# Optimization experiments

Measured on AMD Instinct MI355X. Metric: run time of the kernel, lower is better.

## Reference

```python
import jax, jax.numpy as jnp
import numpy as np

NUM_SKILLS = 50000
HIDDEN = 64
B, T = 8192, 1024
EPS = 1e-6


def setup_inputs() -> dict:
    key = jax.random.key(0)
    ks = jax.random.split(key, 8)
    X = jax.random.randint(ks[0], (B,), 0, NUM_SKILLS)
    y = jax.random.randint(ks[1], (B, T), 0, 2, dtype=jnp.int32)
    embed = jax.random.normal(ks[2], (NUM_SKILLS, HIDDEN), jnp.float32)
    bound = 1.0 / np.sqrt(HIDDEN)
    W0 = jax.random.uniform(ks[3], (HIDDEN, HIDDEN), jnp.float32, -bound, bound)
    b0 = jnp.zeros((HIDDEN,), jnp.float32)
    W1 = jax.random.uniform(ks[4], (HIDDEN, HIDDEN), jnp.float32, -bound, bound)
    b1 = jnp.zeros((HIDDEN,), jnp.float32)
    Wout = jax.random.uniform(ks[5], (HIDDEN, 4), jnp.float32, -bound, bound)
    bout = jnp.zeros((4,), jnp.float32)
    return {"X": X, "y": y, "embed": embed, "W0": W0, "b0": b0,
            "W1": W1, "b1": b1, "Wout": Wout, "bout": bout}


def reference(X, y, embed, W0, b0, W1, b1, Wout, bout):
    # Per-student BKT params from embedding + 2-layer MLP + sigmoid, clamped
    h = embed[X]                                   # (B, H)
    h = jax.nn.relu(h @ W0 + b0)
    h = jax.nn.relu(h @ W1 + b1)
    params = jnp.clip(jax.nn.sigmoid(h @ Wout + bout), EPS, 1.0 - EPS)  # (B, 4)
    l, g, s, prior = params[:, 0], params[:, 1], params[:, 2], params[:, 3]

    def step(latent, y_t):
        true_correct = jnp.where(y_t == -1, 0, y_t)
        correct = latent * (1.0 - s) + (1.0 - latent) * g
        k_t1 = latent * (1.0 - s) / correct
        k_t0 = latent * s / (latent * s + (1.0 - latent) * (1.0 - g))
        k_t = jnp.where(true_correct > 0.5, k_t1, k_t0)
        next_latent = jnp.clip(k_t + (1.0 - k_t) * l, EPS, 1.0 - EPS)
        return next_latent, (correct, latent)

    _, (corrects, latents) = jax.lax.scan(step, prior, y.T)  # scan over T
    return corrects.T, latents.T                            # (B, T) each
```

## Files before the change

kernel.cpp:

```cpp
#include <hip/hip_runtime.h>

#define TSTEPS 1024
#define NROWS  8192
#define CLEN   16
#define KEPS   1e-6f

__device__ __forceinline__ float clampP(float x) {
    return fminf(fmaxf(x, KEPS), 1.f - KEPS);
}
__device__ __forceinline__ float sigm(float v) {
    return 1.0f / (1.0f + __expf(-v));
}

__global__ __launch_bounds__(256) void bkt_params_v4(
    const int* __restrict__ X, const float* __restrict__ embed,
    const float* __restrict__ W0, const float* __restrict__ b0,
    const float* __restrict__ W1, const float* __restrict__ b1,
    const float* __restrict__ Wout, const float* __restrict__ bout,
    float4* __restrict__ params)
{
    const int lane    = threadIdx.x & 63;
    const int wid     = threadIdx.x >> 6;
    const int rowbase = blockIdx.x * 16 + wid * 4;

    __shared__ float sh[4][4][64];
    float (*shw)[64] = sh[wid];

    #pragma unroll
    for (int rs = 0; rs < 4; ++rs) {
        const int skill = X[rowbase + rs];
        shw[rs][lane] = embed[(size_t)skill * 64 + lane];
    }
    __syncthreads();

    float a0 = b0[lane], a1 = a0, a2 = a0, a3 = a0;
    #pragma unroll
    for (int k4 = 0; k4 < 16; ++k4) {
        const float4 e0 = *(const float4*)&shw[0][k4 * 4];
        const float4 e1 = *(const float4*)&shw[1][k4 * 4];
        const float4 e2 = *(const float4*)&shw[2][k4 * 4];
        const float4 e3 = *(const float4*)&shw[3][k4 * 4];
        const float w0 = W0[(k4 * 4 + 0) * 64 + lane];
        const float w1 = W0[(k4 * 4 + 1) * 64 + lane];
        const float w2 = W0[(k4 * 4 + 2) * 64 + lane];
        const float w3 = W0[(k4 * 4 + 3) * 64 + lane];
        a0 = fmaf(e0.x, w0, a0); a0 = fmaf(e0.y, w1, a0); a0 = fmaf(e0.z, w2, a0); a0 = fmaf(e0.w, w3, a0);
        a1 = fmaf(e1.x, w0, a1); a1 = fmaf(e1.y, w1, a1); a1 = fmaf(e1.z, w2, a1); a1 = fmaf(e1.w, w3, a1);
        a2 = fmaf(e2.x, w0, a2); a2 = fmaf(e2.y, w1, a2); a2 = fmaf(e2.z, w2, a2); a2 = fmaf(e2.w, w3, a2);
        a3 = fmaf(e3.x, w0, a3); a3 = fmaf(e3.y, w1, a3); a3 = fmaf(e3.z, w2, a3); a3 = fmaf(e3.w, w3, a3);
    }
    __syncthreads();
    shw[0][lane] = fmaxf(a0, 0.f);
    shw[1][lane] = fmaxf(a1, 0.f);
    shw[2][lane] = fmaxf(a2, 0.f);
    shw[3][lane] = fmaxf(a3, 0.f);
    __syncthreads();

    a0 = b1[lane]; a1 = a0; a2 = a0; a3 = a0;
    #pragma unroll
    for (int k4 = 0; k4 < 16; ++k4) {
        const float4 e0 = *(const float4*)&shw[0][k4 * 4];
        const float4 e1 = *(const float4*)&shw[1][k4 * 4];
        const float4 e2 = *(const float4*)&shw[2][k4 * 4];
        const float4 e3 = *(const float4*)&shw[3][k4 * 4];
        const float w0 = W1[(k4 * 4 + 0) * 64 + lane];
        const float w1 = W1[(k4 * 4 + 1) * 64 + lane];
        const float w2 = W1[(k4 * 4 + 2) * 64 + lane];
        const float w3 = W1[(k4 * 4 + 3) * 64 + lane];
        a0 = fmaf(e0.x, w0, a0); a0 = fmaf(e0.y, w1, a0); a0 = fmaf(e0.z, w2, a0); a0 = fmaf(e0.w, w3, a0);
        a1 = fmaf(e1.x, w0, a1); a1 = fmaf(e1.y, w1, a1); a1 = fmaf(e1.z, w2, a1); a1 = fmaf(e1.w, w3, a1);
        a2 = fmaf(e2.x, w0, a2); a2 = fmaf(e2.y, w1, a2); a2 = fmaf(e2.z, w2, a2); a2 = fmaf(e2.w, w3, a2);
        a3 = fmaf(e3.x, w0, a3); a3 = fmaf(e3.y, w1, a3); a3 = fmaf(e3.z, w2, a3); a3 = fmaf(e3.w, w3, a3);
    }
    const float h0r = fmaxf(a0, 0.f), h1r = fmaxf(a1, 0.f);
    const float h2r = fmaxf(a2, 0.f), h3r = fmaxf(a3, 0.f);

    const float4 wo = ((const float4*)Wout)[lane];
    float p[4][4];
    p[0][0] = h0r * wo.x; p[0][1] = h0r * wo.y; p[0][2] = h0r * wo.z; p[0][3] = h0r * wo.w;
    p[1][0] = h1r * wo.x; p[1][1] = h1r * wo.y; p[1][2] = h1r * wo.z; p[1][3] = h1r * wo.w;
    p[2][0] = h2r * wo.x; p[2][1] = h2r * wo.y; p[2][2] = h2r * wo.z; p[2][3] = h2r * wo.w;
    p[3][0] = h3r * wo.x; p[3][1] = h3r * wo.y; p[3][2] = h3r * wo.z; p[3][3] = h3r * wo.w;
    #pragma unroll
    for (int off = 32; off >= 1; off >>= 1) {
        #pragma unroll
        for (int rs = 0; rs < 4; ++rs)
            #pragma unroll
            for (int c = 0; c < 4; ++c)
                p[rs][c] += __shfl_xor(p[rs][c], off, 64);
    }
    const float4 bo = *(const float4*)bout;
    float v0 = (lane == 0) ? p[0][0] : (lane == 1) ? p[1][0] : (lane == 2) ? p[2][0] : p[3][0];
    float v1 = (lane == 0) ? p[0][1] : (lane == 1) ? p[1][1] : (lane == 2) ? p[2][1] : p[3][1];
    float v2 = (lane == 0) ? p[0][2] : (lane == 1) ? p[1][2] : (lane == 2) ? p[2][2] : p[3][2];
    float v3 = (lane == 0) ? p[0][3] : (lane == 1) ? p[1][3] : (lane == 2) ? p[2][3] : p[3][3];
    if (lane < 4) {
        float4 r;
        r.x = clampP(sigm(v0 + bo.x));
        r.y = clampP(sigm(v1 + bo.y));
        r.z = clampP(sigm(v2 + bo.z));
        r.w = clampP(sigm(v3 + bo.w));
        params[rowbase + lane] = r;
    }
}

__global__ __launch_bounds__(256) void bkt_scan_v4(
    const int* __restrict__ y, const float4* __restrict__ params,
    float* __restrict__ out_corr, float* __restrict__ out_lat)
{
    const int lane = threadIdx.x & 63;
    const int row  = blockIdx.x * 4 + (threadIdx.x >> 6);

    const float4 p = params[row];
    const float l = p.x, g = p.y, s = p.z, prior = p.w;

    const int4* yb = (const int4*)(y + (size_t)row * TSTEPS + lane * CLEN);
    const int4 v0 = yb[0], v1 = yb[1], v2 = yb[2], v3 = yb[3];
    unsigned msk = 0;
    msk |= (v0.x > 0) ? 1u << 0  : 0u; msk |= (v0.y > 0) ? 1u << 1  : 0u;
    msk |= (v0.z > 0) ? 1u << 2  : 0u; msk |= (v0.w > 0) ? 1u << 3  : 0u;
    msk |= (v1.x > 0) ? 1u << 4  : 0u; msk |= (v1.y > 0) ? 1u << 5  : 0u;
    msk |= (v1.z > 0) ? 1u << 6  : 0u; msk |= (v1.w > 0) ? 1u << 7  : 0u;
    msk |= (v2.x > 0) ? 1u << 8  : 0u; msk |= (v2.y > 0) ? 1u << 9  : 0u;
    msk |= (v2.z > 0) ? 1u << 10 : 0u; msk |= (v2.w > 0) ? 1u << 11 : 0u;
    msk |= (v3.x > 0) ? 1u << 12 : 0u; msk |= (v3.y > 0) ? 1u << 13 : 0u;
    msk |= (v3.z > 0) ? 1u << 14 : 0u; msk |= (v3.w > 0) ? 1u << 15 : 0u;

    const float c1 = 1.f - s - g, d1 = g;
    const float e00_1 = fmaf(l, c1, (1.f - l) * (1.f - s));
    const float e01_1 = l * d1;
    const float c0 = s + g - 1.f, d0 = 1.f - g;
    const float e00_0 = fmaf(l, c0, (1.f - l) * s);
    const float e01_0 = l * d0;

    float m00 = 1.f, m01 = 0.f, m10 = 0.f, m11 = 1.f;
    #pragma unroll
    for (int t = 0; t < CLEN; ++t) {
        const bool one = (msk >> t) & 1u;
        const float e00 = one ? e00_1 : e00_0;
        const float e01 = one ? e01_1 : e01_0;
        const float e10 = one ? c1 : c0;
        const float e11 = one ? d1 : d0;
        const float n00 = fmaf(e00, m00, e01 * m10);
        const float n01 = fmaf(e00, m01, e01 * m11);
        const float n10 = fmaf(e10, m00, e11 * m10);
        const float n11 = fmaf(e10, m01, e11 * m11);
        if ((t & 3) == 3) {
            const float inv = __builtin_amdgcn_rcpf(n11);
            m00 = n00 * inv; m01 = n01 * inv; m10 = n10 * inv; m11 = 1.f;
        } else {
            m00 = n00; m01 = n01; m10 = n10; m11 = n11;
        }
    }

    float s00 = m00, s01 = m01, s10 = m10, s11 = m11;
    #pragma unroll
    for (int d = 1; d < 64; d <<= 1) {
        const float t00 = __shfl_up(s00, d, 64);
        const float t01 = __shfl_up(s01, d, 64);
        const float t10 = __shfl_up(s10, d, 64);
        const float t11 = __shfl_up(s11, d, 64);
        if (lane >= d) {
            const float r00 = fmaf(s00, t00, s01 * t10);
            const float r01 = fmaf(s00, t01, s01 * t11);
            const float r10 = fmaf(s10, t00, s11 * t10);
            const float r11 = fmaf(s10, t01, s11 * t11);
            const float inv = __builtin_amdgcn_rcpf(r11);
            s00 = r00 * inv; s01 = r01 * inv; s10 = r10 * inv; s11 = 1.f;
        }
    }
    const float x00 = __shfl_up(s00, 1, 64);
    const float x01 = __shfl_up(s01, 1, 64);
    const float x10 = __shfl_up(s10, 1, 64);
    const float x11 = __shfl_up(s11, 1, 64);
    float L0;
    if (lane == 0) {
        L0 = prior;
    } else {
        const float num = fmaf(x00, prior, x01);
        const float den = fmaf(x10, prior, x11);
        L0 = clampP(num * __builtin_amdgcn_rcpf(den));
    }

    const float a   = 1.f - s;
    const float omg = 1.f - g;
    const float oml = 1.f - l;
    float* oc = out_corr + (size_t)row * TSTEPS + lane * CLEN;
    float* ol = out_lat  + (size_t)row * TSTEPS + lane * CLEN;
    float Lc = L0;
    #pragma unroll
    for (int w = 0; w < 4; ++w) {
        float cr[4], lt[4];
        #pragma unroll
        for (int q = 0; q < 4; ++q) {
            const int t = w * 4 + q;
            const float correct = fmaf(Lc, c1, g);
            const float den0    = fmaf(Lc, c0, omg);
            const float k1 = (Lc * a) * __builtin_amdgcn_rcpf(correct);
            const float k0 = (Lc * s) * __builtin_amdgcn_rcpf(den0);
            const bool one = (msk >> t) & 1u;
            const float k = one ? k1 : k0;
            cr[q] = correct;
            lt[q] = Lc;
            Lc = clampP(fmaf(k, oml, l));
        }
        *(float4*)(oc + w * 4) = make_float4(cr[0], cr[1], cr[2], cr[3]);
        *(float4*)(ol + w * 4) = make_float4(lt[0], lt[1], lt[2], lt[3]);
    }
}

extern "C" void kernel_launch(void* const* d_in, const int* in_sizes, int n_in,
                              void* d_out, int out_size, void* d_ws, size_t ws_size,
                              hipStream_t stream) {
    const int*   X     = (const int*)  d_in[0];
    const int*   y     = (const int*)  d_in[1];
    const float* embed = (const float*)d_in[2];
    const float* W0    = (const float*)d_in[3];
    const float* b0    = (const float*)d_in[4];
    const float* W1    = (const float*)d_in[5];
    const float* b1    = (const float*)d_in[6];
    const float* Wout  = (const float*)d_in[7];
    const float* bout  = (const float*)d_in[8];

    float* out_corr = (float*)d_out;
    float* out_lat  = out_corr + (size_t)NROWS * TSTEPS;
    float4* paramsb = (float4*)d_ws;

    bkt_params_v4<<<NROWS / 16, 256, 0, stream>>>(X, embed, W0, b0, W1, b1, Wout, bout, paramsb);
    bkt_scan_v4 <<<NROWS / 4,  256, 0, stream>>>(y, paramsb, out_corr, out_lat);
}
```

Baseline: 134.0 us.

## Coalesce y loads via ballots and stage outputs through LDS for coalesced stores

Each lane used to load 16 contiguous ints and write 16 contiguous floats, so a wavefront's accesses were strided by 64 bytes. Now y is read with coalesced int4 loads across the wave, and __ballot plus bit shuffling rebuilds each lane's 16-bit correctness mask. Outputs are staged in padded shared memory (stride 17 to avoid bank conflicts) and written back as fully coalesced float4 stores. The cost is 34 KB of LDS per block, which may limit occupancy, plus a block-wide __syncthreads where only per-wave sync is needed.

```diff
diff --git a/kernel.cpp b/kernel.cpp
--- a/kernel.cpp
+++ b/kernel.cpp
@@ -104,27 +104,43 @@
     }
 }
 
-__global__ __launch_bounds__(256) void bkt_scan_v4(
+__global__ __launch_bounds__(256) void bkt_scan_v5(
     const int* __restrict__ y, const float4* __restrict__ params,
     float* __restrict__ out_corr, float* __restrict__ out_lat)
 {
     const int lane = threadIdx.x & 63;
-    const int row  = blockIdx.x * 4 + (threadIdx.x >> 6);
+    const int wid  = threadIdx.x >> 6;
+    const int row  = blockIdx.x * 4 + wid;
+
+    __shared__ float shbuf[4][2][64 * 17];
+    float* shc = shbuf[wid][0];
+    float* shl = shbuf[wid][1];
 
     const float4 p = params[row];
     const float l = p.x, g = p.y, s = p.z, prior = p.w;
 
-    const int4* yb = (const int4*)(y + (size_t)row * TSTEPS + lane * CLEN);
-    const int4 v0 = yb[0], v1 = yb[1], v2 = yb[2], v3 = yb[3];
+    const int4* yrow = (const int4*)(y + (size_t)row * TSTEPS);
+    unsigned long long B[4][4];
+    #pragma unroll
+    for (int j = 0; j < 4; ++j) {
+        const int4 v = yrow[j * 64 + lane];
+        B[j][0] = __ballot(v.x > 0);
+        B[j][1] = __ballot(v.y > 0);
+        B[j][2] = __ballot(v.z > 0);
+        B[j][3] = __ballot(v.w > 0);
+    }
+    const int jsel  = lane >> 4;
+    const int ibase = (lane & 15) * 4;
     unsigned msk = 0;
-    msk |= (v0.x > 0) ? 1u << 0  : 0u; msk |= (v0.y > 0) ? 1u << 1  : 0u;
-    msk |= (v0.z > 0) ? 1u << 2  : 0u; msk |= (v0.w > 0) ? 1u << 3  : 0u;
-    msk |= (v1.x > 0) ? 1u << 4  : 0u; msk |= (v1.y > 0) ? 1u << 5  : 0u;
-    msk |= (v1.z > 0) ? 1u << 6  : 0u; msk |= (v1.w > 0) ? 1u << 7  : 0u;
-    msk |= (v2.x > 0) ? 1u << 8  : 0u; msk |= (v2.y > 0) ? 1u << 9  : 0u;
-    msk |= (v2.z > 0) ? 1u << 10 : 0u; msk |= (v2.w > 0) ? 1u << 11 : 0u;
-    msk |= (v3.x > 0) ? 1u << 12 : 0u; msk |= (v3.y > 0) ? 1u << 13 : 0u;
-    msk |= (v3.z > 0) ? 1u << 14 : 0u; msk |= (v3.w > 0) ? 1u << 15 : 0u;
+    #pragma unroll
+    for (int e = 0; e < 4; ++e) {
+        const unsigned long long be =
+            (jsel == 0) ? B[0][e] : (jsel == 1) ? B[1][e] :
+            (jsel == 2) ? B[2][e] : B[3][e];
+        const unsigned n  = (unsigned)(be >> ibase) & 0xFu;
+        const unsigned sp = (n & 1u) | ((n & 2u) << 3) | ((n & 4u) << 6) | ((n & 8u) << 9);
+        msk |= sp << e;
+    }
 
     const float c1 = 1.f - s - g, d1 = g;
     const float e00_1 = fmaf(l, c1, (1.f - l) * (1.f - s));
@@ -185,27 +201,40 @@
     const float a   = 1.f - s;
     const float omg = 1.f - g;
     const float oml = 1.f - l;
-    float* oc = out_corr + (size_t)row * TSTEPS + lane * CLEN;
-    float* ol = out_lat  + (size_t)row * TSTEPS + lane * CLEN;
+    float cr[CLEN], lt[CLEN];
     float Lc = L0;
     #pragma unroll
-    for (int w = 0; w < 4; ++w) {
-        float cr[4], lt[4];
-        #pragma unroll
-        for (int q = 0; q < 4; ++q) {
-            const int t = w * 4 + q;
-            const float correct = fmaf(Lc, c1, g);
-            const float den0    = fmaf(Lc, c0, omg);
-            const float k1 = (Lc * a) * __builtin_amdgcn_rcpf(correct);
-            const float k0 = (Lc * s) * __builtin_amdgcn_rcpf(den0);
-            const bool one = (msk >> t) & 1u;
-            const float k = one ? k1 : k0;
-            cr[q] = correct;
-            lt[q] = Lc;
-            Lc = clampP(fmaf(k, oml, l));
-        }
-        *(float4*)(oc + w * 4) = make_float4(cr[0], cr[1], cr[2], cr[3]);
-        *(float4*)(ol + w * 4) = make_float4(lt[0], lt[1], lt[2], lt[3]);
+    for (int t = 0; t < CLEN; ++t) {
+        const float correct = fmaf(Lc, c1, g);
+        const float den0    = fmaf(Lc, c0, omg);
+        const float k1 = (Lc * a) * __builtin_amdgcn_rcpf(correct);
+        const float k0 = (Lc * s) * __builtin_amdgcn_rcpf(den0);
+        const bool one = (msk >> t) & 1u;
+        const float k = one ? k1 : k0;
+        cr[t] = correct;
+        lt[t] = Lc;
+        Lc = clampP(fmaf(k, oml, l));
+    }
+
+    #pragma unroll
+    for (int t = 0; t < CLEN; ++t) {
+        shc[lane * 17 + t] = cr[t];
+        shl[lane * 17 + t] = lt[t];
+    }
+    __syncthreads();
+
+    float* oc = out_corr + (size_t)row * TSTEPS;
+    float* ol = out_lat  + (size_t)row * TSTEPS;
+    #pragma unroll
+    for (int j = 0; j < 4; ++j) {
+        const int c    = j * 16 + (lane >> 2);
+        const int q    = (lane & 3) * 4;
+        const int base = c * 17 + q;
+        float4 vc, vl;
+        vc.x = shc[base + 0]; vc.y = shc[base + 1]; vc.z = shc[base + 2]; vc.w = shc[base + 3];
+        vl.x = shl[base + 0]; vl.y = shl[base + 1]; vl.z = shl[base + 2]; vl.w = shl[base + 3];
+        *(float4*)(oc + j * 256 + lane * 4) = vc;
+        *(float4*)(ol + j * 256 + lane * 4) = vl;
     }
 }
 
@@ -227,5 +256,5 @@
     float4* paramsb = (float4*)d_ws;
 
     bkt_params_v4<<<NROWS / 16, 256, 0, stream>>>(X, embed, W0, b0, W1, b1, Wout, bout, paramsb);
-    bkt_scan_v4 <<<NROWS / 4,  256, 0, stream>>>(y, paramsb, out_corr, out_lat);
-}
+    bkt_scan_v5 <<<NROWS / 4,  256, 0, stream>>>(y, paramsb, out_corr, out_lat);
+}
```

New measurement: 123.9 us. 7.5% less time.
